# Performance work log

Hardware: AMD Instinct MI355X
Metric: run time of the kernel (lower is better)

Reference implementation:

```python
import jax, jax.numpy as jnp
import numpy as np

TEMP = 0.07


def setup_inputs() -> dict:
    key = jax.random.key(0)
    k1, k2 = jax.random.split(key)
    N, C = 8192, 512
    X = jax.random.normal(k1, (N, C), dtype=jnp.float32)
    Y = jax.random.normal(k2, (N, C), dtype=jnp.float32)
    return {"X": X, "Y": Y}


def reference(X, Y):
    # Original loop computes, per row i, cross-entropy over logits
    # [X_i.Y_i, X_i.Y_j (j != i)] / temp with label 0 (the positive).
    # Softmax CE is permutation-invariant, so this equals
    #   logsumexp(S_i / temp) - S_ii / temp,  S = X @ Y^T,
    # summed over rows (loop accumulates with +=, i.e. sum reduction).
    S = jnp.einsum('nc,mc->nm', X, Y) / TEMP  # [N, N]
    lse = jax.nn.logsumexp(S, axis=1)          # [N]
    pos = jnp.diagonal(S)                      # [N]
    return jnp.sum(lse - pos)
```

## Files before the change

kernel.cpp:

```cpp
#include <hip/hip_runtime.h>
#include <stdint.h>

#define N 8192
#define C 512
#define BM 128
#define BN 128
#define BKF 128
#define NSPLIT 8
#define COLS_PER_SPLIT (N / NSPLIT)
#define CT (COLS_PER_SPLIT / BN)
#define GRID_GEMM (64 * NSPLIT)
#define INV_T 14.285714285714286f

typedef __attribute__((ext_vector_type(4)))  int   i32x4;
typedef __attribute__((ext_vector_type(8)))  int   i32x8;
typedef __attribute__((ext_vector_type(16))) float f32x16;

__global__ __launch_bounds__(256) void prep_kernel(const float* __restrict__ X,
                                                   const float* __restrict__ Y,
                                                   unsigned char* __restrict__ Xf8,
                                                   unsigned char* __restrict__ Yf8,
                                                   float* __restrict__ pos) {
  const int wave = threadIdx.x >> 6;
  const int lane = threadIdx.x & 63;
  const int row = blockIdx.x * 4 + wave;
  const float4* xr = (const float4*)(X + (size_t)row * C) + lane * 2;
  const float4* yr = (const float4*)(Y + (size_t)row * C) + lane * 2;
  float4 x0 = xr[0], x1 = xr[1];
  float4 y0 = yr[0], y1 = yr[1];
  float s = x0.x * y0.x + x0.y * y0.y + x0.z * y0.z + x0.w * y0.w
          + x1.x * y1.x + x1.y * y1.y + x1.z * y1.z + x1.w * y1.w;
  int2 ox, oy;
  ox.x = __builtin_amdgcn_cvt_pk_fp8_f32(x0.x, x0.y, 0, false);
  ox.x = __builtin_amdgcn_cvt_pk_fp8_f32(x0.z, x0.w, ox.x, true);
  ox.y = __builtin_amdgcn_cvt_pk_fp8_f32(x1.x, x1.y, 0, false);
  ox.y = __builtin_amdgcn_cvt_pk_fp8_f32(x1.z, x1.w, ox.y, true);
  oy.x = __builtin_amdgcn_cvt_pk_fp8_f32(y0.x, y0.y, 0, false);
  oy.x = __builtin_amdgcn_cvt_pk_fp8_f32(y0.z, y0.w, oy.x, true);
  oy.y = __builtin_amdgcn_cvt_pk_fp8_f32(y1.x, y1.y, 0, false);
  oy.y = __builtin_amdgcn_cvt_pk_fp8_f32(y1.z, y1.w, oy.y, true);
  ((int2*)(Xf8 + (size_t)row * C))[lane] = ox;
  ((int2*)(Yf8 + (size_t)row * C))[lane] = oy;
#pragma unroll
  for (int off = 32; off >= 1; off >>= 1) s += __shfl_xor(s, off);
  if (lane == 0) pos[row] = s * INV_T;
}

__global__ __launch_bounds__(256, 2) void gemm_lse_kernel(const unsigned char* __restrict__ Xf8,
                                                          const unsigned char* __restrict__ Yf8,
                                                          float2* __restrict__ partials) {
  __shared__ unsigned char Bs[2][BN][BKF];

  const int tid = threadIdx.x;
  const int bx = blockIdx.x;
  const int split = bx & (NSPLIT - 1);
  const int rb = bx >> 3;
  const int row0 = rb * BM;
  const int colbase = split * COLS_PER_SPLIT;

  const int w = tid >> 6;
  const int lane = tid & 63;
  const int lrow = lane & 31;
  const int h = lane >> 5;
  const int arow = w * 32 + lrow;
  const int swz = lrow & 7;

  i32x4 aLo[8], aHi[8];
  {
    const unsigned char* abase = Xf8 + (size_t)(row0 + arow) * C + h * 32;
#pragma unroll
    for (int kk = 0; kk < 8; ++kk) {
      asm volatile("global_load_dwordx4 %0, %1, off"
                   : "=v"(aLo[kk]) : "v"(abase + kk * 64));
      asm volatile("global_load_dwordx4 %0, %1, off offset:16"
                   : "=v"(aHi[kk]) : "v"(abase + kk * 64));
    }
  }

  const int r_base = tid >> 3;
  const int p = tid & 7;
  const int j = p ^ (r_base & 7);

  auto stageB = [&](int buf, int col0, int k0) {
#pragma unroll
    for (int i = 0; i < 4; ++i) {
      const int r = i * 32 + r_base;
      const unsigned char* gb = Yf8 + (size_t)(col0 + r) * C + k0 * BKF + j * 16;
      uint32_t loff = (uint32_t)((i * 256 + (tid & ~63)) * 16);
      __builtin_amdgcn_global_load_lds(
          (const __attribute__((address_space(1))) uint32_t*)(uintptr_t)gb,
          (__attribute__((address_space(3))) uint32_t*)(uintptr_t)((char*)&Bs[buf][0][0] + loff),
          16, 0, 0);
    }
  };

  stageB(0, colbase, 0);
  asm volatile("s_waitcnt vmcnt(0)" ::: "memory");
  __builtin_amdgcn_sched_barrier(0);
  __builtin_amdgcn_s_barrier();
  __builtin_amdgcn_sched_barrier(0);

  float m_s[16], l_s[16];
#pragma unroll
  for (int s = 0; s < 16; ++s) { m_s[s] = -INFINITY; l_s[s] = 0.0f; }

  for (int ct = 0; ct < CT; ++ct) {
    f32x16 acc[4];
#pragma unroll
    for (int t = 0; t < 4; ++t)
#pragma unroll
      for (int e = 0; e < 16; ++e) acc[t][e] = 0.0f;

#pragma unroll
    for (int k0 = 0; k0 < 4; ++k0) {
      const int nct = (k0 == 3) ? ((ct + 1) & (CT - 1)) : ct;
      const int nk0 = (k0 + 1) & 3;
      stageB((k0 + 1) & 1, colbase + nct * BN, nk0);
      __builtin_amdgcn_sched_barrier(0);
      asm volatile("s_waitcnt vmcnt(4)" ::: "memory");
      __builtin_amdgcn_s_barrier();
      __builtin_amdgcn_sched_barrier(0);

      __builtin_amdgcn_s_setprio(1);
#pragma unroll
      for (int s = 0; s < 2; ++s) {
        const int kk = 2 * k0 + s;
        i32x8 af = { aLo[kk][0], aLo[kk][1], aLo[kk][2], aLo[kk][3],
                     aHi[kk][0], aHi[kk][1], aHi[kk][2], aHi[kk][3] };
        const int c0 = 4 * s + 2 * h;
#pragma unroll
        for (int tj = 0; tj < 4; ++tj) {
          const int brow = tj * 32 + lrow;
          i32x4 blo = *(const i32x4*)&Bs[k0 & 1][brow][((c0    ) ^ swz) * 16];
          i32x4 bhi = *(const i32x4*)&Bs[k0 & 1][brow][((c0 + 1) ^ swz) * 16];
          i32x8 bf = { blo[0], blo[1], blo[2], blo[3], bhi[0], bhi[1], bhi[2], bhi[3] };
          acc[tj] = __builtin_amdgcn_mfma_scale_f32_32x32x64_f8f6f4(
              af, bf, acc[tj], 0, 0, 0, 127, 0, 127);
        }
      }
      __builtin_amdgcn_s_setprio(0);
      __builtin_amdgcn_sched_barrier(0);
      __builtin_amdgcn_s_barrier();
      __builtin_amdgcn_sched_barrier(0);
    }

#pragma unroll
    for (int r = 0; r < 16; ++r) {
      float v0 = acc[0][r] * INV_T;
      float v1 = acc[1][r] * INV_T;
      float v2 = acc[2][r] * INV_T;
      float v3 = acc[3][r] * INV_T;
      float mx = fmaxf(fmaxf(v0, v1), fmaxf(v2, v3));
      float mn = fmaxf(m_s[r], mx);
      l_s[r] = l_s[r] * __expf(m_s[r] - mn)
             + __expf(v0 - mn) + __expf(v1 - mn) + __expf(v2 - mn) + __expf(v3 - mn);
      m_s[r] = mn;
    }
  }

  asm volatile("s_waitcnt vmcnt(0)" ::: "memory");

#pragma unroll
  for (int r = 0; r < 16; ++r) {
    float m = m_s[r], l = l_s[r];
#pragma unroll
    for (int off = 1; off < 32; off <<= 1) {
      float mo = __shfl_xor(m, off);
      float lo = __shfl_xor(l, off);
      float mn = fmaxf(m, mo);
      l = l * __expf(m - mn) + lo * __expf(mo - mn);
      m = mn;
    }
    m_s[r] = m; l_s[r] = l;
  }
  if (lrow == 0) {
#pragma unroll
    for (int r = 0; r < 16; ++r) {
      int row_local = (r & 3) + 8 * (r >> 2) + 4 * h;
      partials[(size_t)split * N + (row0 + w * 32 + row_local)] =
          make_float2(m_s[r], l_s[r]);
    }
  }
}

__global__ __launch_bounds__(256) void combine_kernel(const float2* __restrict__ partials,
                                                      const float* __restrict__ pos,
                                                      float* __restrict__ out) {
  int row = blockIdx.x * 256 + threadIdx.x;
  float M = -INFINITY, L = 0.0f;
#pragma unroll
  for (int s = 0; s < NSPLIT; ++s) {
    float2 pr = partials[(size_t)s * N + row];
    float mn = fmaxf(M, pr.x);
    L = L * __expf(M - mn) + pr.y * __expf(pr.x - mn);
    M = mn;
  }
  float v = M + __logf(L) - pos[row];
#pragma unroll
  for (int off = 32; off >= 1; off >>= 1) v += __shfl_xor(v, off);
  __shared__ float wsum[4];
  if ((threadIdx.x & 63) == 0) wsum[threadIdx.x >> 6] = v;
  __syncthreads();
  if (threadIdx.x == 0) atomicAdd(out, wsum[0] + wsum[1] + wsum[2] + wsum[3]);
}

extern "C" void kernel_launch(void* const* d_in, const int* in_sizes, int n_in,
                              void* d_out, int out_size, void* d_ws, size_t ws_size,
                              hipStream_t stream) {
  const float* X = (const float*)d_in[0];
  const float* Y = (const float*)d_in[1];
  float* out = (float*)d_out;

  char* w = (char*)d_ws;
  unsigned char* Xf8 = (unsigned char*)w;
  unsigned char* Yf8 = Xf8 + (size_t)N * C;
  float2* partials = (float2*)(Yf8 + (size_t)N * C);
  float* pos = (float*)((char*)partials + (size_t)NSPLIT * N * sizeof(float2));

  hipMemsetAsync(d_out, 0, sizeof(float), stream);
  prep_kernel<<<N / 4, 256, 0, stream>>>(X, Y, Xf8, Yf8, pos);
  gemm_lse_kernel<<<GRID_GEMM, 256, 0, stream>>>(Xf8, Yf8, partials);
  combine_kernel<<<N / 256, 256, 0, stream>>>(partials, pos, out);
}
```

Measured before the change: 122.0 us.

## Double row tile per block and fuse combine into GEMM via last-block counter

Doubles the row tile to 256 so each wave holds two A fragments in registers and reuses each B fragment from shared memory for two MFMAs. This halves B-tile traffic per output and halves the grid, at the cost of dropping occupancy to one block per CU. The separate combine kernel and the memset are removed: the last of the splits to finish a row block, found through an atomic counter, merges the partials and adds to the output, and the prep kernel zeroes the counters and the output. The risks are register pressure from doubled accumulators and fewer blocks to hide latency.

```diff
diff --git a/kernel.cpp b/kernel.cpp
--- a/kernel.cpp
+++ b/kernel.cpp
@@ -3,13 +3,13 @@
 
 #define N 8192
 #define C 512
-#define BM 128
+#define BM 256
 #define BN 128
 #define BKF 128
 #define NSPLIT 8
 #define COLS_PER_SPLIT (N / NSPLIT)
 #define CT (COLS_PER_SPLIT / BN)
-#define GRID_GEMM (64 * NSPLIT)
+#define GRID_GEMM ((N / BM) * NSPLIT)
 #define INV_T 14.285714285714286f
 
 typedef __attribute__((ext_vector_type(4)))  int   i32x4;
@@ -20,7 +20,13 @@
                                                    const float* __restrict__ Y,
                                                    unsigned char* __restrict__ Xf8,
                                                    unsigned char* __restrict__ Yf8,
-                                                   float* __restrict__ pos) {
+                                                   float* __restrict__ pos,
+                                                   int* __restrict__ cnt,
+                                                   float* __restrict__ out) {
+  if (blockIdx.x == 0) {
+    if (threadIdx.x < (N / BM)) cnt[threadIdx.x] = 0;
+    if (threadIdx.x == 64) *out = 0.0f;
+  }
   const int wave = threadIdx.x >> 6;
   const int lane = threadIdx.x & 63;
   const int row = blockIdx.x * 4 + wave;
@@ -46,10 +52,15 @@
   if (lane == 0) pos[row] = s * INV_T;
 }
 
-__global__ __launch_bounds__(256, 2) void gemm_lse_kernel(const unsigned char* __restrict__ Xf8,
+__global__ __launch_bounds__(256, 1) void gemm_lse_kernel(const unsigned char* __restrict__ Xf8,
                                                           const unsigned char* __restrict__ Yf8,
-                                                          float2* __restrict__ partials) {
+                                                          float2* __restrict__ partials,
+                                                          const float* __restrict__ pos,
+                                                          int* __restrict__ cnt,
+                                                          float* __restrict__ out) {
   __shared__ unsigned char Bs[2][BN][BKF];
+  __shared__ float wsum[4];
+  __shared__ int mflag;
 
   const int tid = threadIdx.x;
   const int bx = blockIdx.x;
@@ -62,18 +73,22 @@
   const int lane = tid & 63;
   const int lrow = lane & 31;
   const int h = lane >> 5;
-  const int arow = w * 32 + lrow;
   const int swz = lrow & 7;
 
-  i32x4 aLo[8], aHi[8];
+  i32x4 tL0[8], tH0[8], tL1[8], tH1[8];
   {
-    const unsigned char* abase = Xf8 + (size_t)(row0 + arow) * C + h * 32;
+    const unsigned char* a0 = Xf8 + (size_t)(row0 + w * 64 + lrow) * C + h * 32;
+    const unsigned char* a1 = a0 + (size_t)32 * C;
 #pragma unroll
     for (int kk = 0; kk < 8; ++kk) {
       asm volatile("global_load_dwordx4 %0, %1, off"
-                   : "=v"(aLo[kk]) : "v"(abase + kk * 64));
+                   : "=v"(tL0[kk]) : "v"(a0 + kk * 64));
       asm volatile("global_load_dwordx4 %0, %1, off offset:16"
-                   : "=v"(aHi[kk]) : "v"(abase + kk * 64));
+                   : "=v"(tH0[kk]) : "v"(a0 + kk * 64));
+      asm volatile("global_load_dwordx4 %0, %1, off"
+                   : "=v"(tL1[kk]) : "v"(a1 + kk * 64));
+      asm volatile("global_load_dwordx4 %0, %1, off offset:16"
+                   : "=v"(tH1[kk]) : "v"(a1 + kk * 64));
     }
   }
 
@@ -100,16 +115,28 @@
   __builtin_amdgcn_s_barrier();
   __builtin_amdgcn_sched_barrier(0);
 
-  float m_s[16], l_s[16];
-#pragma unroll
-  for (int s = 0; s < 16; ++s) { m_s[s] = -INFINITY; l_s[s] = 0.0f; }
+  i32x8 aF0[8], aF1[8];
+#pragma unroll
+  for (int kk = 0; kk < 8; ++kk) {
+    aF0[kk] = (i32x8){ tL0[kk][0], tL0[kk][1], tL0[kk][2], tL0[kk][3],
+                       tH0[kk][0], tH0[kk][1], tH0[kk][2], tH0[kk][3] };
+    aF1[kk] = (i32x8){ tL1[kk][0], tL1[kk][1], tL1[kk][2], tL1[kk][3],
+                       tH1[kk][0], tH1[kk][1], tH1[kk][2], tH1[kk][3] };
+  }
+
+  float m0[16], l0[16], m1[16], l1[16];
+#pragma unroll
+  for (int s = 0; s < 16; ++s) {
+    m0[s] = -INFINITY; l0[s] = 0.0f;
+    m1[s] = -INFINITY; l1[s] = 0.0f;
+  }
 
   for (int ct = 0; ct < CT; ++ct) {
-    f32x16 acc[4];
+    f32x16 acc0[4], acc1[4];
 #pragma unroll
     for (int t = 0; t < 4; ++t)
 #pragma unroll
-      for (int e = 0; e < 16; ++e) acc[t][e] = 0.0f;
+      for (int e = 0; e < 16; ++e) { acc0[t][e] = 0.0f; acc1[t][e] = 0.0f; }
 
 #pragma unroll
     for (int k0 = 0; k0 < 4; ++k0) {
@@ -125,8 +152,6 @@
 #pragma unroll
       for (int s = 0; s < 2; ++s) {
         const int kk = 2 * k0 + s;
-        i32x8 af = { aLo[kk][0], aLo[kk][1], aLo[kk][2], aLo[kk][3],
-                     aHi[kk][0], aHi[kk][1], aHi[kk][2], aHi[kk][3] };
         const int c0 = 4 * s + 2 * h;
 #pragma unroll
         for (int tj = 0; tj < 4; ++tj) {
@@ -134,8 +159,10 @@
           i32x4 blo = *(const i32x4*)&Bs[k0 & 1][brow][((c0    ) ^ swz) * 16];
           i32x4 bhi = *(const i32x4*)&Bs[k0 & 1][brow][((c0 + 1) ^ swz) * 16];
           i32x8 bf = { blo[0], blo[1], blo[2], blo[3], bhi[0], bhi[1], bhi[2], bhi[3] };
-          acc[tj] = __builtin_amdgcn_mfma_scale_f32_32x32x64_f8f6f4(
-              af, bf, acc[tj], 0, 0, 0, 127, 0, 127);
+          acc0[tj] = __builtin_amdgcn_mfma_scale_f32_32x32x64_f8f6f4(
+              aF0[kk], bf, acc0[tj], 0, 0, 0, 127, 0, 127);
+          acc1[tj] = __builtin_amdgcn_mfma_scale_f32_32x32x64_f8f6f4(
+              aF1[kk], bf, acc1[tj], 0, 0, 0, 127, 0, 127);
         }
       }
       __builtin_amdgcn_s_setprio(0);
@@ -146,15 +173,24 @@
 
 #pragma unroll
     for (int r = 0; r < 16; ++r) {
-      float v0 = acc[0][r] * INV_T;
-      float v1 = acc[1][r] * INV_T;
-      float v2 = acc[2][r] * INV_T;
-      float v3 = acc[3][r] * INV_T;
-      float mx = fmaxf(fmaxf(v0, v1), fmaxf(v2, v3));
-      float mn = fmaxf(m_s[r], mx);
-      l_s[r] = l_s[r] * __expf(m_s[r] - mn)
-             + __expf(v0 - mn) + __expf(v1 - mn) + __expf(v2 - mn) + __expf(v3 - mn);
-      m_s[r] = mn;
+      {
+        float v0 = acc0[0][r] * INV_T, v1 = acc0[1][r] * INV_T;
+        float v2 = acc0[2][r] * INV_T, v3 = acc0[3][r] * INV_T;
+        float mx = fmaxf(fmaxf(v0, v1), fmaxf(v2, v3));
+        float mn = fmaxf(m0[r], mx);
+        l0[r] = l0[r] * __expf(m0[r] - mn)
+              + __expf(v0 - mn) + __expf(v1 - mn) + __expf(v2 - mn) + __expf(v3 - mn);
+        m0[r] = mn;
+      }
+      {
+        float v0 = acc1[0][r] * INV_T, v1 = acc1[1][r] * INV_T;
+        float v2 = acc1[2][r] * INV_T, v3 = acc1[3][r] * INV_T;
+        float mx = fmaxf(fmaxf(v0, v1), fmaxf(v2, v3));
+        float mn = fmaxf(m1[r], mx);
+        l1[r] = l1[r] * __expf(m1[r] - mn)
+              + __expf(v0 - mn) + __expf(v1 - mn) + __expf(v2 - mn) + __expf(v3 - mn);
+        m1[r] = mn;
+      }
     }
   }
 
@@ -162,46 +198,55 @@
 
 #pragma unroll
   for (int r = 0; r < 16; ++r) {
-    float m = m_s[r], l = l_s[r];
+    float ma = m0[r], la = l0[r], mb = m1[r], lb = l1[r];
 #pragma unroll
     for (int off = 1; off < 32; off <<= 1) {
-      float mo = __shfl_xor(m, off);
-      float lo = __shfl_xor(l, off);
-      float mn = fmaxf(m, mo);
-      l = l * __expf(m - mn) + lo * __expf(mo - mn);
-      m = mn;
-    }
-    m_s[r] = m; l_s[r] = l;
+      float mo = __shfl_xor(ma, off), lo = __shfl_xor(la, off);
+      float mn = fmaxf(ma, mo);
+      la = la * __expf(ma - mn) + lo * __expf(mo - mn);
+      ma = mn;
+      float mo2 = __shfl_xor(mb, off), lo2 = __shfl_xor(lb, off);
+      float mn2 = fmaxf(mb, mo2);
+      lb = lb * __expf(mb - mn2) + lo2 * __expf(mo2 - mn2);
+      mb = mn2;
+    }
+    m0[r] = ma; l0[r] = la; m1[r] = mb; l1[r] = lb;
   }
   if (lrow == 0) {
 #pragma unroll
     for (int r = 0; r < 16; ++r) {
       int row_local = (r & 3) + 8 * (r >> 2) + 4 * h;
-      partials[(size_t)split * N + (row0 + w * 32 + row_local)] =
-          make_float2(m_s[r], l_s[r]);
-    }
-  }
-}
-
-__global__ __launch_bounds__(256) void combine_kernel(const float2* __restrict__ partials,
-                                                      const float* __restrict__ pos,
-                                                      float* __restrict__ out) {
-  int row = blockIdx.x * 256 + threadIdx.x;
-  float M = -INFINITY, L = 0.0f;
-#pragma unroll
-  for (int s = 0; s < NSPLIT; ++s) {
-    float2 pr = partials[(size_t)s * N + row];
-    float mn = fmaxf(M, pr.x);
-    L = L * __expf(M - mn) + pr.y * __expf(pr.x - mn);
-    M = mn;
-  }
-  float v = M + __logf(L) - pos[row];
-#pragma unroll
-  for (int off = 32; off >= 1; off >>= 1) v += __shfl_xor(v, off);
-  __shared__ float wsum[4];
-  if ((threadIdx.x & 63) == 0) wsum[threadIdx.x >> 6] = v;
+      int base = row0 + w * 64;
+      partials[(size_t)split * N + (base + row_local)]      = make_float2(m0[r], l0[r]);
+      partials[(size_t)split * N + (base + 32 + row_local)] = make_float2(m1[r], l1[r]);
+    }
+  }
+
   __syncthreads();
-  if (threadIdx.x == 0) atomicAdd(out, wsum[0] + wsum[1] + wsum[2] + wsum[3]);
+  if (tid == 0) {
+    __threadfence();
+    int old = atomicAdd(&cnt[rb], 1);
+    mflag = (old == NSPLIT - 1) ? 1 : 0;
+  }
+  __syncthreads();
+  if (mflag) {
+    __threadfence();
+    int row = row0 + tid;
+    float M = -INFINITY, L = 0.0f;
+#pragma unroll
+    for (int s = 0; s < NSPLIT; ++s) {
+      float2 pr = partials[(size_t)s * N + row];
+      float mn = fmaxf(M, pr.x);
+      L = L * __expf(M - mn) + pr.y * __expf(pr.x - mn);
+      M = mn;
+    }
+    float v = M + __logf(L) - pos[row];
+#pragma unroll
+    for (int off = 32; off >= 1; off >>= 1) v += __shfl_xor(v, off);
+    if (lane == 0) wsum[w] = v;
+    __syncthreads();
+    if (tid == 0) atomicAdd(out, wsum[0] + wsum[1] + wsum[2] + wsum[3]);
+  }
 }
 
 extern "C" void kernel_launch(void* const* d_in, const int* in_sizes, int n_in,
@@ -216,9 +261,8 @@
   unsigned char* Yf8 = Xf8 + (size_t)N * C;
   float2* partials = (float2*)(Yf8 + (size_t)N * C);
   float* pos = (float*)((char*)partials + (size_t)NSPLIT * N * sizeof(float2));
-
-  hipMemsetAsync(d_out, 0, sizeof(float), stream);
-  prep_kernel<<<N / 4, 256, 0, stream>>>(X, Y, Xf8, Yf8, pos);
-  gemm_lse_kernel<<<GRID_GEMM, 256, 0, stream>>>(Xf8, Yf8, partials);
-  combine_kernel<<<N / 256, 256, 0, stream>>>(partials, pos, out);
+  int* cnt = (int*)(pos + N);
+
+  prep_kernel<<<N / 4, 256, 0, stream>>>(X, Y, Xf8, Yf8, pos, cnt, out);
+  gemm_lse_kernel<<<GRID_GEMM, 256, 0, stream>>>(Xf8, Yf8, partials, pos, cnt, out);
 }
```

After: 140.2 us. 14.9% more time.

## Deepen B-tile prefetch to four LDS buffers and fuse combine into GEMM

Applied to the files above, without the earlier changes.

The LDS staging for Y tiles grows from double to quad buffering, so loads are issued three k-steps ahead with a looser vmcnt wait. The separate combine kernel and the memset are removed: prep zeroes the counters and output, and the last GEMM block per row-band (found via an atomic counter) merges the partial logsumexps and adds to the output. This saves launch overhead and hides global latency, at the cost of doubled LDS use (64KB per block), which may limit occupancy.

```diff
diff --git a/kernel.cpp b/kernel.cpp
--- a/kernel.cpp
+++ b/kernel.cpp
@@ -9,7 +9,9 @@
 #define NSPLIT 8
 #define COLS_PER_SPLIT (N / NSPLIT)
 #define CT (COLS_PER_SPLIT / BN)
-#define GRID_GEMM (64 * NSPLIT)
+#define NRB (N / BM)
+#define GRID_GEMM (NRB * NSPLIT)
+#define NTILES (CT * 4)
 #define INV_T 14.285714285714286f
 
 typedef __attribute__((ext_vector_type(4)))  int   i32x4;
@@ -20,7 +22,13 @@
                                                    const float* __restrict__ Y,
                                                    unsigned char* __restrict__ Xf8,
                                                    unsigned char* __restrict__ Yf8,
-                                                   float* __restrict__ pos) {
+                                                   float* __restrict__ pos,
+                                                   int* __restrict__ cnt,
+                                                   float* __restrict__ out) {
+  if (blockIdx.x == 0) {
+    if (threadIdx.x < NRB) cnt[threadIdx.x] = 0;
+    if (threadIdx.x == 64 + NRB) *out = 0.0f;
+  }
   const int wave = threadIdx.x >> 6;
   const int lane = threadIdx.x & 63;
   const int row = blockIdx.x * 4 + wave;
@@ -48,8 +56,13 @@
 
 __global__ __launch_bounds__(256, 2) void gemm_lse_kernel(const unsigned char* __restrict__ Xf8,
                                                           const unsigned char* __restrict__ Yf8,
-                                                          float2* __restrict__ partials) {
-  __shared__ unsigned char Bs[2][BN][BKF];
+                                                          float2* __restrict__ partials,
+                                                          const float* __restrict__ pos,
+                                                          int* __restrict__ cnt,
+                                                          float* __restrict__ out) {
+  __shared__ unsigned char Bs[4][BN][BKF];
+  __shared__ float wsum[4];
+  __shared__ int mflag;
 
   const int tid = threadIdx.x;
   const int bx = blockIdx.x;
@@ -65,15 +78,15 @@
   const int arow = w * 32 + lrow;
   const int swz = lrow & 7;
 
-  i32x4 aLo[8], aHi[8];
+  i32x4 tLo[8], tHi[8];
   {
     const unsigned char* abase = Xf8 + (size_t)(row0 + arow) * C + h * 32;
 #pragma unroll
     for (int kk = 0; kk < 8; ++kk) {
       asm volatile("global_load_dwordx4 %0, %1, off"
-                   : "=v"(aLo[kk]) : "v"(abase + kk * 64));
+                   : "=v"(tLo[kk]) : "v"(abase + kk * 64));
       asm volatile("global_load_dwordx4 %0, %1, off offset:16"
-                   : "=v"(aHi[kk]) : "v"(abase + kk * 64));
+                   : "=v"(tHi[kk]) : "v"(abase + kk * 64));
     }
   }
 
@@ -86,20 +99,28 @@
     for (int i = 0; i < 4; ++i) {
       const int r = i * 32 + r_base;
       const unsigned char* gb = Yf8 + (size_t)(col0 + r) * C + k0 * BKF + j * 16;
-      uint32_t loff = (uint32_t)((i * 256 + (tid & ~63)) * 16);
+      uint32_t loff = (uint32_t)(buf * (BN * BKF) + (i * 256 + (tid & ~63)) * 16);
       __builtin_amdgcn_global_load_lds(
           (const __attribute__((address_space(1))) uint32_t*)(uintptr_t)gb,
-          (__attribute__((address_space(3))) uint32_t*)(uintptr_t)((char*)&Bs[buf][0][0] + loff),
+          (__attribute__((address_space(3))) uint32_t*)(uintptr_t)((char*)&Bs[0][0][0] + loff),
           16, 0, 0);
     }
   };
 
   stageB(0, colbase, 0);
+  stageB(1, colbase, 1);
+  stageB(2, colbase, 2);
   asm volatile("s_waitcnt vmcnt(0)" ::: "memory");
   __builtin_amdgcn_sched_barrier(0);
   __builtin_amdgcn_s_barrier();
   __builtin_amdgcn_sched_barrier(0);
 
+  i32x8 aF[8];
+#pragma unroll
+  for (int kk = 0; kk < 8; ++kk)
+    aF[kk] = (i32x8){ tLo[kk][0], tLo[kk][1], tLo[kk][2], tLo[kk][3],
+                      tHi[kk][0], tHi[kk][1], tHi[kk][2], tHi[kk][3] };
+
   float m_s[16], l_s[16];
 #pragma unroll
   for (int s = 0; s < 16; ++s) { m_s[s] = -INFINITY; l_s[s] = 0.0f; }
@@ -113,11 +134,11 @@
 
 #pragma unroll
     for (int k0 = 0; k0 < 4; ++k0) {
-      const int nct = (k0 == 3) ? ((ct + 1) & (CT - 1)) : ct;
-      const int nk0 = (k0 + 1) & 3;
-      stageB((k0 + 1) & 1, colbase + nct * BN, nk0);
-      __builtin_amdgcn_sched_barrier(0);
-      asm volatile("s_waitcnt vmcnt(4)" ::: "memory");
+      const int tl3 = ct * 4 + k0 + 3;
+      const int tl = (tl3 < NTILES - 1) ? tl3 : (NTILES - 1);
+      stageB((k0 + 3) & 3, colbase + (tl >> 2) * BN, tl & 3);
+      __builtin_amdgcn_sched_barrier(0);
+      asm volatile("s_waitcnt vmcnt(12)" ::: "memory");
       __builtin_amdgcn_s_barrier();
       __builtin_amdgcn_sched_barrier(0);
 
@@ -125,17 +146,17 @@
 #pragma unroll
       for (int s = 0; s < 2; ++s) {
         const int kk = 2 * k0 + s;
-        i32x8 af = { aLo[kk][0], aLo[kk][1], aLo[kk][2], aLo[kk][3],
-                     aHi[kk][0], aHi[kk][1], aHi[kk][2], aHi[kk][3] };
         const int c0 = 4 * s + 2 * h;
 #pragma unroll
         for (int tj = 0; tj < 4; ++tj) {
           const int brow = tj * 32 + lrow;
-          i32x4 blo = *(const i32x4*)&Bs[k0 & 1][brow][((c0    ) ^ swz) * 16];
-          i32x4 bhi = *(const i32x4*)&Bs[k0 & 1][brow][((c0 + 1) ^ swz) * 16];
-          i32x8 bf = { blo[0], blo[1], blo[2], blo[3], bhi[0], bhi[1], bhi[2], bhi[3] };
+          i32x8 bf;
+          *(i32x4*)&bf =
+              *(const i32x4*)&Bs[k0][brow][((c0    ) ^ swz) * 16];
+          *(((i32x4*)&bf) + 1) =
+              *(const i32x4*)&Bs[k0][brow][((c0 + 1) ^ swz) * 16];
           acc[tj] = __builtin_amdgcn_mfma_scale_f32_32x32x64_f8f6f4(
-              af, bf, acc[tj], 0, 0, 0, 127, 0, 127);
+              aF[kk], bf, acc[tj], 0, 0, 0, 127, 0, 127);
         }
       }
       __builtin_amdgcn_s_setprio(0);
@@ -181,27 +202,35 @@
           make_float2(m_s[r], l_s[r]);
     }
   }
-}
-
-__global__ __launch_bounds__(256) void combine_kernel(const float2* __restrict__ partials,
-                                                      const float* __restrict__ pos,
-                                                      float* __restrict__ out) {
-  int row = blockIdx.x * 256 + threadIdx.x;
-  float M = -INFINITY, L = 0.0f;
-#pragma unroll
-  for (int s = 0; s < NSPLIT; ++s) {
-    float2 pr = partials[(size_t)s * N + row];
-    float mn = fmaxf(M, pr.x);
-    L = L * __expf(M - mn) + pr.y * __expf(pr.x - mn);
-    M = mn;
-  }
-  float v = M + __logf(L) - pos[row];
-#pragma unroll
-  for (int off = 32; off >= 1; off >>= 1) v += __shfl_xor(v, off);
-  __shared__ float wsum[4];
-  if ((threadIdx.x & 63) == 0) wsum[threadIdx.x >> 6] = v;
+
   __syncthreads();
-  if (threadIdx.x == 0) atomicAdd(out, wsum[0] + wsum[1] + wsum[2] + wsum[3]);
+  if (tid == 0) {
+    __threadfence();
+    int old = atomicAdd(&cnt[rb], 1);
+    mflag = (old == NSPLIT - 1) ? 1 : 0;
+  }
+  __syncthreads();
+  if (mflag) {
+    __threadfence();
+    float v = 0.0f;
+    if (tid < BM) {
+      const int row = row0 + tid;
+      float M = -INFINITY, L = 0.0f;
+#pragma unroll
+      for (int s = 0; s < NSPLIT; ++s) {
+        float2 pr = partials[(size_t)s * N + row];
+        float mn = fmaxf(M, pr.x);
+        L = L * __expf(M - mn) + pr.y * __expf(pr.x - mn);
+        M = mn;
+      }
+      v = M + __logf(L) - pos[row];
+    }
+#pragma unroll
+    for (int off = 32; off >= 1; off >>= 1) v += __shfl_xor(v, off);
+    if (lane == 0) wsum[w] = v;
+    __syncthreads();
+    if (tid == 0) atomicAdd(out, wsum[0] + wsum[1] + wsum[2] + wsum[3]);
+  }
 }
 
 extern "C" void kernel_launch(void* const* d_in, const int* in_sizes, int n_in,
@@ -216,9 +245,8 @@
   unsigned char* Yf8 = Xf8 + (size_t)N * C;
   float2* partials = (float2*)(Yf8 + (size_t)N * C);
   float* pos = (float*)((char*)partials + (size_t)NSPLIT * N * sizeof(float2));
-
-  hipMemsetAsync(d_out, 0, sizeof(float), stream);
-  prep_kernel<<<N / 4, 256, 0, stream>>>(X, Y, Xf8, Yf8, pos);
-  gemm_lse_kernel<<<GRID_GEMM, 256, 0, stream>>>(Xf8, Yf8, partials);
-  combine_kernel<<<N / 256, 256, 0, stream>>>(partials, pos, out);
+  int* cnt = (int*)(pos + N);
+
+  prep_kernel<<<N / 4, 256, 0, stream>>>(X, Y, Xf8, Yf8, pos, cnt, out);
+  gemm_lse_kernel<<<GRID_GEMM, 256, 0, stream>>>(Xf8, Yf8, partials, pos, cnt, out);
 }
```

After: 134.7 us. +10.4%, slower.
